# Kernel optimization log

Hardware: AMD Instinct MI355X
Metric: run time of the kernel (lower is better)

The kernel has to match this reference:

```python
import jax, jax.numpy as jnp
import numpy as np

N = 50000      # nodes
E = 800000     # directed edges
D = 128        # input_dim == hidden_dim
EL = 100000    # edges scored by decoder


def setup_inputs() -> dict:
    key = jax.random.key(0)
    ks = jax.random.split(key, 8)
    s = 1.0 / np.sqrt(D)  # glorot-ish scale
    return {
        "node_feature": jax.random.normal(ks[0], (N, D), jnp.float32),
        "W1": jax.random.normal(ks[1], (D, D), jnp.float32) * s,
        "b1": jnp.zeros((D,), jnp.float32),
        "W2": jax.random.normal(ks[2], (D, D), jnp.float32) * s,
        "b2": jnp.zeros((D,), jnp.float32),
        "W3": jax.random.normal(ks[3], (D, D), jnp.float32) * s,
        "b3": jnp.zeros((D,), jnp.float32),
        "edge_index": jax.random.randint(ks[4], (2, E), 0, N, dtype=jnp.int32),
        "edge_label_index": jax.random.randint(ks[5], (2, EL), 0, N, dtype=jnp.int32),
    }


def _gcn_conv(x, W, b, src, dst, norm, n):
    # x' = D^{-1/2} (A + I) D^{-1/2} (x W) + b   (PyG GCNConv semantics)
    h = x @ W                                   # [N, D]
    msg = h[src] * norm[:, None]                # gather + scale, [E+N, D]
    out = jax.ops.segment_sum(msg, dst, num_segments=n)  # scatter-add
    return out + b


def reference(node_feature, W1, b1, W2, b2, W3, b3, edge_index, edge_label_index):
    n = node_feature.shape[0]
    loop = jnp.arange(n, dtype=edge_index.dtype)
    src = jnp.concatenate([edge_index[0], loop])  # self-loops appended
    dst = jnp.concatenate([edge_index[1], loop])
    # symmetric normalization: deg over destinations (incl. self-loops)
    deg = jax.ops.segment_sum(jnp.ones_like(dst, dtype=node_feature.dtype), dst, num_segments=n)
    dinv = jax.lax.rsqrt(jnp.maximum(deg, 1.0))
    norm = dinv[src] * dinv[dst]                 # [E+N]

    x = jax.nn.relu(_gcn_conv(node_feature, W1, b1, src, dst, norm, n))
    x = jax.nn.relu(_gcn_conv(x, W2, b2, src, dst, norm, n))
    x = _gcn_conv(x, W3, b3, src, dst, norm, n)

    # dot-product edge decoder
    u = x[edge_label_index[0]]
    v = x[edge_label_index[1]]
    return jnp.sum(u * v, axis=-1)               # [EL] logits
```

## Files before the change

kernel.cpp:

```cpp
#include <hip/hip_runtime.h>
#include <hip/hip_bf16.h>
#include <hip/hip_fp16.h>

typedef _Float16 v8h __attribute__((ext_vector_type(8)));
typedef _Float16 v4h __attribute__((ext_vector_type(4)));
typedef float v4f __attribute__((ext_vector_type(4)));

__global__ __launch_bounds__(256) void wswz(const float* __restrict__ W1,
                                            const float* __restrict__ W2,
                                            const float* __restrict__ W3,
                                            __half* __restrict__ wfrag) {
    int o = blockIdx.x * 256 + threadIdx.x;
    int w = o >> 14, r = o & 16383;
    const float* Ws = (w >= 3) ? W3 : ((w == 2) ? W2 : W1);
    float v = Ws[r];
    __half h;
    if (w == 1) {
        __half hv = __float2half_rn(v);
        h = __float2half_rn(v - __half2float(hv));
    } else {
        h = __float2half_rn(v);
    }
    int k = r >> 7, ncol = r & 127;
    int c = ncol >> 4, nl = ncol & 15;
    int s = k >> 5, quad = (k >> 3) & 3, j = k & 7;
    int di = ((c * 4 + s) * 64 + quad * 16 + nl) * 8 + j;
    wfrag[(size_t)w * 16384 + di] = h;
}

__global__ __launch_bounds__(256) void gemm1_mfma(const float* __restrict__ X,
                                                  const __half* __restrict__ wfrag,
                                                  __half* __restrict__ H, int Nrows,
                                                  int degBlocks,
                                                  const int* __restrict__ dst,
                                                  int* __restrict__ cnt,
                                                  int* __restrict__ rank, int E) {
    int tid = threadIdx.x;
    if (blockIdx.x < degBlocks) {
        int base = blockIdx.x * 2048 + tid * 8;
        if (base + 7 < E) {
            int4 d0 = *(const int4*)&dst[base];
            int4 d1 = *(const int4*)&dst[base + 4];
            int r0 = atomicAdd(&cnt[d0.x * 16], 1);
            int r1 = atomicAdd(&cnt[d0.y * 16], 1);
            int r2 = atomicAdd(&cnt[d0.z * 16], 1);
            int r3 = atomicAdd(&cnt[d0.w * 16], 1);
            int r4 = atomicAdd(&cnt[d1.x * 16], 1);
            int r5 = atomicAdd(&cnt[d1.y * 16], 1);
            int r6 = atomicAdd(&cnt[d1.z * 16], 1);
            int r7 = atomicAdd(&cnt[d1.w * 16], 1);
            *(int4*)&rank[base]     = make_int4(r0, r1, r2, r3);
            *(int4*)&rank[base + 4] = make_int4(r4, r5, r6, r7);
        } else {
            for (int e = base; e < E; ++e) rank[e] = atomicAdd(&cnt[dst[e] * 16], 1);
        }
        return;
    }
    int gb = blockIdx.x - degBlocks;
    int rowbase = gb * 64;
    int l = tid & 63;
    int wid = tid >> 6;
    int rb = wid * 16;
    int quad = l >> 4;
    int nn = l & 15;
    int gr = rowbase + rb + nn;
    v8h ah[4], al[4];
    if (gr < Nrows) {
        const float* Xr = &X[(size_t)gr * 128 + quad * 8];
#pragma unroll
        for (int k = 0; k < 4; ++k) {
            float4 f0 = *(const float4*)&Xr[k * 32];
            float4 f1 = *(const float4*)&Xr[k * 32 + 4];
            float ff[8] = {f0.x, f0.y, f0.z, f0.w, f1.x, f1.y, f1.z, f1.w};
            v8h h, lo;
#pragma unroll
            for (int m = 0; m < 8; ++m) {
                _Float16 hv = (_Float16)ff[m];
                h[m] = hv;
                lo[m] = (_Float16)(ff[m] - (float)hv);
            }
            ah[k] = h;
            al[k] = lo;
        }
    } else {
#pragma unroll
        for (int k = 0; k < 4; ++k) {
            v8h z;
#pragma unroll
            for (int m = 0; m < 8; ++m) z[m] = (_Float16)0.f;
            ah[k] = z;
            al[k] = z;
        }
    }
    const v8h* Wh = (const v8h*)wfrag;
    const v8h* Wl = (const v8h*)(wfrag + 16384);
    v4f acc[8] = {};
#pragma unroll
    for (int c = 0; c < 8; ++c) {
        v8h bh0 = Wh[(c * 4 + 0) * 64 + l];
        v8h bh1 = Wh[(c * 4 + 1) * 64 + l];
        v8h bh2 = Wh[(c * 4 + 2) * 64 + l];
        v8h bh3 = Wh[(c * 4 + 3) * 64 + l];
        acc[c] = __builtin_amdgcn_mfma_f32_16x16x32_f16(ah[0], bh0, acc[c], 0, 0, 0);
        acc[c] = __builtin_amdgcn_mfma_f32_16x16x32_f16(ah[1], bh1, acc[c], 0, 0, 0);
        acc[c] = __builtin_amdgcn_mfma_f32_16x16x32_f16(ah[2], bh2, acc[c], 0, 0, 0);
        acc[c] = __builtin_amdgcn_mfma_f32_16x16x32_f16(ah[3], bh3, acc[c], 0, 0, 0);
        acc[c] = __builtin_amdgcn_mfma_f32_16x16x32_f16(al[0], bh0, acc[c], 0, 0, 0);
        acc[c] = __builtin_amdgcn_mfma_f32_16x16x32_f16(al[1], bh1, acc[c], 0, 0, 0);
        acc[c] = __builtin_amdgcn_mfma_f32_16x16x32_f16(al[2], bh2, acc[c], 0, 0, 0);
        acc[c] = __builtin_amdgcn_mfma_f32_16x16x32_f16(al[3], bh3, acc[c], 0, 0, 0);
        v8h bl0 = Wl[(c * 4 + 0) * 64 + l];
        v8h bl1 = Wl[(c * 4 + 1) * 64 + l];
        v8h bl2 = Wl[(c * 4 + 2) * 64 + l];
        v8h bl3 = Wl[(c * 4 + 3) * 64 + l];
        acc[c] = __builtin_amdgcn_mfma_f32_16x16x32_f16(ah[0], bl0, acc[c], 0, 0, 0);
        acc[c] = __builtin_amdgcn_mfma_f32_16x16x32_f16(ah[1], bl1, acc[c], 0, 0, 0);
        acc[c] = __builtin_amdgcn_mfma_f32_16x16x32_f16(ah[2], bl2, acc[c], 0, 0, 0);
        acc[c] = __builtin_amdgcn_mfma_f32_16x16x32_f16(ah[3], bl3, acc[c], 0, 0, 0);
    }
#pragma unroll
    for (int reg = 0; reg < 4; ++reg) {
        int grr = rowbase + rb + quad * 4 + reg;
        if (grr < Nrows) {
#pragma unroll
            for (int c = 0; c < 8; ++c)
                H[(size_t)grr * 128 + c * 16 + nn] = __float2half_rn(acc[c][reg]);
        }
    }
}

__global__ __launch_bounds__(256) void agg_gemm(const __half* __restrict__ Xs,
                                                const float* __restrict__ dinv,
                                                const int* __restrict__ rowptr,
                                                const int* __restrict__ col,
                                                const __half* __restrict__ wfrag,
                                                const float* __restrict__ bias,
                                                __half* __restrict__ Out,
                                                int n, int finalLayer) {
    __shared__ __align__(16) _Float16 y[64][136];
    int tid = threadIdx.x;
    int rowbase = blockIdx.x * 64;
    {
        int sub = tid >> 4;
        int t = (tid & 15) * 8;
        for (int g = 0; g < 4; ++g) {
            int rr = g * 16 + sub;
            int node = rowbase + rr;
            float a[8] = {};
            if (node < n) {
                int beg = rowptr[node], end = rowptr[node + 1];
                int k = beg;
                for (; k + 4 <= end; k += 4) {
                    int s0 = col[k], s1 = col[k + 1], s2 = col[k + 2], s3 = col[k + 3];
                    uint4 r0 = *(const uint4*)&Xs[(size_t)s0 * 128 + t];
                    uint4 r1 = *(const uint4*)&Xs[(size_t)s1 * 128 + t];
                    uint4 r2 = *(const uint4*)&Xs[(size_t)s2 * 128 + t];
                    uint4 r3 = *(const uint4*)&Xs[(size_t)s3 * 128 + t];
                    const __half2* h0 = (const __half2*)&r0;
                    const __half2* h1 = (const __half2*)&r1;
                    const __half2* h2 = (const __half2*)&r2;
                    const __half2* h3 = (const __half2*)&r3;
#pragma unroll
                    for (int m = 0; m < 4; ++m) {
                        float2 f0 = __half22float2(h0[m]);
                        float2 f1 = __half22float2(h1[m]);
                        float2 f2 = __half22float2(h2[m]);
                        float2 f3 = __half22float2(h3[m]);
                        a[2 * m]     += (f0.x + f1.x) + (f2.x + f3.x);
                        a[2 * m + 1] += (f0.y + f1.y) + (f2.y + f3.y);
                    }
                }
                for (; k < end; ++k) {
                    uint4 r0 = *(const uint4*)&Xs[(size_t)col[k] * 128 + t];
                    const __half2* h0 = (const __half2*)&r0;
#pragma unroll
                    for (int m = 0; m < 4; ++m) {
                        float2 f0 = __half22float2(h0[m]);
                        a[2 * m] += f0.x;
                        a[2 * m + 1] += f0.y;
                    }
                }
                float dn = dinv[node];
#pragma unroll
                for (int m = 0; m < 8; ++m) a[m] *= dn;
            }
            v8h yv;
#pragma unroll
            for (int m = 0; m < 8; ++m) yv[m] = (_Float16)a[m];
            *(v8h*)&y[rr][t] = yv;
        }
    }
    __syncthreads();
    int l = tid & 63;
    int wid = tid >> 6;
    int rb = wid * 16;
    int quad = l >> 4;
    int nn = l & 15;
    v8h a0 = *(const v8h*)&y[rb + nn][0 * 32 + quad * 8];
    v8h a1 = *(const v8h*)&y[rb + nn][1 * 32 + quad * 8];
    v8h a2 = *(const v8h*)&y[rb + nn][2 * 32 + quad * 8];
    v8h a3 = *(const v8h*)&y[rb + nn][3 * 32 + quad * 8];
    const v8h* Wf = (const v8h*)wfrag;
    v4f acc[8] = {};
#pragma unroll
    for (int c = 0; c < 8; ++c) {
        v8h b0 = Wf[(c * 4 + 0) * 64 + l];
        v8h b1 = Wf[(c * 4 + 1) * 64 + l];
        v8h b2 = Wf[(c * 4 + 2) * 64 + l];
        v8h b3 = Wf[(c * 4 + 3) * 64 + l];
        acc[c] = __builtin_amdgcn_mfma_f32_16x16x32_f16(a0, b0, acc[c], 0, 0, 0);
        acc[c] = __builtin_amdgcn_mfma_f32_16x16x32_f16(a1, b1, acc[c], 0, 0, 0);
        acc[c] = __builtin_amdgcn_mfma_f32_16x16x32_f16(a2, b2, acc[c], 0, 0, 0);
        acc[c] = __builtin_amdgcn_mfma_f32_16x16x32_f16(a3, b3, acc[c], 0, 0, 0);
    }
#pragma unroll
    for (int reg = 0; reg < 4; ++reg) {
        int gr = rowbase + rb + quad * 4 + reg;
        if (gr < n) {
            float dn = dinv[gr];
#pragma unroll
            for (int c = 0; c < 8; ++c) {
                float z = acc[c][reg] + bias[c * 16 + nn];
                if (!finalLayer) z = fmaxf(z, 0.f) * dn;
                Out[(size_t)gr * 128 + c * 16 + nn] = __float2half_rn(z);
            }
        }
    }
}

__global__ void scanA(const int* __restrict__ cnt, int* __restrict__ tmp,
                      int* __restrict__ bsum, int n) {
    __shared__ int s[256];
    int i = blockIdx.x * 256 + threadIdx.x;
    int v = (i < n) ? (cnt[i * 16] + 1) : 0;
    s[threadIdx.x] = v;
    __syncthreads();
    for (int off = 1; off < 256; off <<= 1) {
        int x = (threadIdx.x >= off) ? s[threadIdx.x - off] : 0;
        __syncthreads();
        s[threadIdx.x] += x;
        __syncthreads();
    }
    if (i < n) tmp[i] = s[threadIdx.x];
    if (threadIdx.x == 255) bsum[blockIdx.x] = s[255];
}

__global__ void scanB(const int* __restrict__ tmp, const int* __restrict__ bsum,
                      const int* __restrict__ cnt, int* __restrict__ rowptr,
                      float* __restrict__ dinv, int* __restrict__ col, int n, int nb) {
    __shared__ int p[256];
    int t = threadIdx.x;
    p[t] = (t < nb) ? bsum[t] : 0;
    __syncthreads();
    for (int off = 1; off < 256; off <<= 1) {
        int x = (t >= off) ? p[t - off] : 0;
        __syncthreads();
        p[t] += x;
        __syncthreads();
    }
    int prefix = (blockIdx.x == 0) ? 0 : p[blockIdx.x - 1];
    int i = blockIdx.x * 256 + t;
    if (i < n) {
        int inc = tmp[i] + prefix;
        rowptr[i + 1] = inc;
        int c1 = cnt[i * 16] + 1;
        dinv[i] = rsqrtf((float)c1);
        col[inc - c1] = i;
        if (i == 0) rowptr[0] = 0;
    }
}

__global__ __launch_bounds__(256) void fill4(const int* __restrict__ src,
                                             const int* __restrict__ dst,
                                             const int* __restrict__ rank,
                                             const int* __restrict__ rowptr,
                                             int* __restrict__ col, int E) {
    int base = blockIdx.x * 1024 + threadIdx.x * 4;
    if (base + 3 < E) {
        int d0 = dst[base], d1 = dst[base + 1], d2 = dst[base + 2], d3 = dst[base + 3];
        int s0 = src[base], s1 = src[base + 1], s2 = src[base + 2], s3 = src[base + 3];
        int r0 = rank[base], r1 = rank[base + 1], r2 = rank[base + 2], r3 = rank[base + 3];
        col[rowptr[d0] + 1 + r0] = s0;
        col[rowptr[d1] + 1 + r1] = s1;
        col[rowptr[d2] + 1 + r2] = s2;
        col[rowptr[d3] + 1 + r3] = s3;
    } else {
        for (int e = base; e < E; ++e)
            col[rowptr[dst[e]] + 1 + rank[e]] = src[e];
    }
}

__global__ __launch_bounds__(256) void agg_h(const __half* __restrict__ H,
                                             const float* __restrict__ dinv,
                                             const int* __restrict__ rowptr,
                                             const int* __restrict__ col,
                                             const float* __restrict__ bias,
                                             __half* __restrict__ out, int n) {
    int node = blockIdx.x * 16 + (threadIdx.x >> 4);
    int t = (threadIdx.x & 15) * 8;
    if (node >= n) return;
    int beg = rowptr[node], end = rowptr[node + 1];
    float a[8] = {};
    int k = beg;
    for (; k + 4 <= end; k += 4) {
        int s0 = col[k], s1 = col[k + 1], s2 = col[k + 2], s3 = col[k + 3];
        float w0 = dinv[s0], w1 = dinv[s1], w2 = dinv[s2], w3 = dinv[s3];
        uint4 r0 = *(const uint4*)&H[(size_t)s0 * 128 + t];
        uint4 r1 = *(const uint4*)&H[(size_t)s1 * 128 + t];
        uint4 r2 = *(const uint4*)&H[(size_t)s2 * 128 + t];
        uint4 r3 = *(const uint4*)&H[(size_t)s3 * 128 + t];
        const __half2* h0 = (const __half2*)&r0;
        const __half2* h1 = (const __half2*)&r1;
        const __half2* h2 = (const __half2*)&r2;
        const __half2* h3 = (const __half2*)&r3;
#pragma unroll
        for (int m = 0; m < 4; ++m) {
            float2 f0 = __half22float2(h0[m]);
            float2 f1 = __half22float2(h1[m]);
            float2 f2 = __half22float2(h2[m]);
            float2 f3 = __half22float2(h3[m]);
            a[2 * m]     += f0.x * w0 + f1.x * w1 + f2.x * w2 + f3.x * w3;
            a[2 * m + 1] += f0.y * w0 + f1.y * w1 + f2.y * w2 + f3.y * w3;
        }
    }
    for (; k < end; ++k) {
        int s0 = col[k];
        float w0 = dinv[s0];
        uint4 r0 = *(const uint4*)&H[(size_t)s0 * 128 + t];
        const __half2* h0 = (const __half2*)&r0;
#pragma unroll
        for (int m = 0; m < 4; ++m) {
            float2 f0 = __half22float2(h0[m]);
            a[2 * m] += f0.x * w0;
            a[2 * m + 1] += f0.y * w0;
        }
    }
    float dn = dinv[node];
    float4 b0 = *(const float4*)&bias[t];
    float4 b1 = *(const float4*)&bias[t + 4];
    float r0 = fmaxf(a[0] * dn + b0.x, 0.f) * dn;
    float r1 = fmaxf(a[1] * dn + b0.y, 0.f) * dn;
    float r2 = fmaxf(a[2] * dn + b0.z, 0.f) * dn;
    float r3 = fmaxf(a[3] * dn + b0.w, 0.f) * dn;
    float r4 = fmaxf(a[4] * dn + b1.x, 0.f) * dn;
    float r5 = fmaxf(a[5] * dn + b1.y, 0.f) * dn;
    float r6 = fmaxf(a[6] * dn + b1.z, 0.f) * dn;
    float r7 = fmaxf(a[7] * dn + b1.w, 0.f) * dn;
    auto pk = [](float x, float y) { __half2 h = __floats2half2_rn(x, y); return *(unsigned int*)&h; };
    uint4 o = make_uint4(pk(r0, r1), pk(r2, r3), pk(r4, r5), pk(r6, r7));
    *(uint4*)&out[(size_t)node * 128 + t] = o;
}

__global__ __launch_bounds__(256) void decoder_h(const __half* __restrict__ X,
                                                 const int* __restrict__ eli,
                                                 float* __restrict__ out, int EL) {
    int e = blockIdx.x * 16 + (threadIdx.x >> 4);
    int lane = threadIdx.x & 15;
    if (e >= EL) return;
    int u = eli[e], v = eli[EL + e];
    uint4 ra = *(const uint4*)&X[(size_t)u * 128 + lane * 8];
    uint4 rb = *(const uint4*)&X[(size_t)v * 128 + lane * 8];
    const __half2* ha = (const __half2*)&ra;
    const __half2* hb = (const __half2*)&rb;
    float d = 0.f;
#pragma unroll
    for (int j = 0; j < 4; ++j) {
        float2 fa = __half22float2(ha[j]);
        float2 fb = __half22float2(hb[j]);
        d += fa.x * fb.x + fa.y * fb.y;
    }
#pragma unroll
    for (int off = 8; off > 0; off >>= 1) d += __shfl_xor(d, off);
    if (lane == 0) out[e] = d;
}

extern "C" void kernel_launch(void* const* d_in, const int* in_sizes, int n_in,
                              void* d_out, int out_size, void* d_ws, size_t ws_size,
                              hipStream_t stream) {
    const float* x0 = (const float*)d_in[0];
    const float* W1 = (const float*)d_in[1];
    const float* b1 = (const float*)d_in[2];
    const float* W2 = (const float*)d_in[3];
    const float* b2 = (const float*)d_in[4];
    const float* W3 = (const float*)d_in[5];
    const float* b3 = (const float*)d_in[6];
    const int* ei   = (const int*)d_in[7];
    const int* eli  = (const int*)d_in[8];
    float* out = (float*)d_out;

    const int D = 128;
    const int N  = in_sizes[0] / D;
    const int E  = in_sizes[7] / 2;
    const int EL = in_sizes[8] / 2;

    const int* src = ei;
    const int* dst = ei + E;

    char* ws = (char*)d_ws;
    size_t off = 0;
    auto alloc = [&](size_t bytes) -> void* {
        off = (off + 255) & ~(size_t)255;
        void* p = ws + off;
        off += bytes;
        return p;
    };
    int*    cnt    = (int*)alloc((size_t)N * 16 * sizeof(int));
    int*    tmp    = (int*)alloc((size_t)N * sizeof(int));
    int*    bsum   = (int*)alloc(256 * sizeof(int));
    int*    rowptr = (int*)alloc((size_t)(N + 1) * sizeof(int));
    float*  dinv   = (float*)alloc((size_t)N * sizeof(float));
    int*    rank   = (int*)alloc((size_t)E * sizeof(int));
    int*    col    = (int*)alloc((size_t)(E + N) * sizeof(int));
    __half* wfrag  = (__half*)alloc((size_t)4 * 16384 * sizeof(__half));
    __half* hbuf   = (__half*)alloc((size_t)N * D * sizeof(__half));
    __half* xbuf   = (__half*)alloc((size_t)N * D * sizeof(__half));
    (void)ws_size;

    hipMemsetAsync(cnt, 0, (size_t)N * 16 * sizeof(int), stream);

    int nbN = (N + 255) / 256;
    int nbE4 = (E + 1023) / 1024;
    int nbE8 = (E + 2047) / 2048;
    int gemmGrid = (N + 63) / 64;
    int fusedGrid = (N + 63) / 64;
    int aggGrid  = (N + 15) / 16;

    wswz<<<256, 256, 0, stream>>>(W1, W2, W3, wfrag);

    gemm1_mfma<<<nbE8 + gemmGrid, 256, 0, stream>>>(x0, wfrag, hbuf, N,
                                                    nbE8, dst, cnt, rank, E);

    scanA<<<nbN, 256, 0, stream>>>(cnt, tmp, bsum, N);
    scanB<<<nbN, 256, 0, stream>>>(tmp, bsum, cnt, rowptr, dinv, col, N, nbN);
    fill4<<<nbE4, 256, 0, stream>>>(src, dst, rank, rowptr, col, E);

    agg_h<<<aggGrid, 256, 0, stream>>>(hbuf, dinv, rowptr, col, b1, xbuf, N);
    agg_gemm<<<fusedGrid, 256, 0, stream>>>(xbuf, dinv, rowptr, col, wfrag + 2 * 16384, b2, hbuf, N, 0);
    agg_gemm<<<fusedGrid, 256, 0, stream>>>(hbuf, dinv, rowptr, col, wfrag + 3 * 16384, b3, xbuf, N, 1);

    decoder_h<<<(EL + 15) / 16, 256, 0, stream>>>(xbuf, eli, out, EL);
}
```

Baseline: 266.5 us.

## Use wavefront-per-node aggregation, compact degree counters, prefetch weight fragments

The aggregation kernels now assign a full 64-lane wavefront to each node, with each lane loading one half2 and the edge loop unrolled by 8. This replaces the previous scheme of 16 lanes per node with uint4 loads, aiming for more edge-level memory parallelism and better balance across node degrees. The degree counter array drops its 16-int padding, which shrinks the memset and the scan reads at the risk of more atomic contention within a cache line. The first GEMM also prefetches the next column group's high weight fragments while the current MFMAs run.

```diff
diff --git a/kernel.cpp b/kernel.cpp
--- a/kernel.cpp
+++ b/kernel.cpp
@@ -28,36 +28,35 @@
     wfrag[(size_t)w * 16384 + di] = h;
 }
 
-__global__ __launch_bounds__(256) void gemm1_mfma(const float* __restrict__ X,
-                                                  const __half* __restrict__ wfrag,
-                                                  __half* __restrict__ H, int Nrows,
-                                                  int degBlocks,
-                                                  const int* __restrict__ dst,
-                                                  int* __restrict__ cnt,
-                                                  int* __restrict__ rank, int E) {
+__global__ __launch_bounds__(256) void gemm1_deg(const float* __restrict__ X,
+                                                 const __half* __restrict__ wfrag,
+                                                 __half* __restrict__ H, int Nrows,
+                                                 int degBlocks,
+                                                 const int* __restrict__ dst,
+                                                 int* __restrict__ cnt,
+                                                 int* __restrict__ rank, int E) {
     int tid = threadIdx.x;
     if (blockIdx.x < degBlocks) {
         int base = blockIdx.x * 2048 + tid * 8;
         if (base + 7 < E) {
             int4 d0 = *(const int4*)&dst[base];
             int4 d1 = *(const int4*)&dst[base + 4];
-            int r0 = atomicAdd(&cnt[d0.x * 16], 1);
-            int r1 = atomicAdd(&cnt[d0.y * 16], 1);
-            int r2 = atomicAdd(&cnt[d0.z * 16], 1);
-            int r3 = atomicAdd(&cnt[d0.w * 16], 1);
-            int r4 = atomicAdd(&cnt[d1.x * 16], 1);
-            int r5 = atomicAdd(&cnt[d1.y * 16], 1);
-            int r6 = atomicAdd(&cnt[d1.z * 16], 1);
-            int r7 = atomicAdd(&cnt[d1.w * 16], 1);
+            int r0 = atomicAdd(&cnt[d0.x], 1);
+            int r1 = atomicAdd(&cnt[d0.y], 1);
+            int r2 = atomicAdd(&cnt[d0.z], 1);
+            int r3 = atomicAdd(&cnt[d0.w], 1);
+            int r4 = atomicAdd(&cnt[d1.x], 1);
+            int r5 = atomicAdd(&cnt[d1.y], 1);
+            int r6 = atomicAdd(&cnt[d1.z], 1);
+            int r7 = atomicAdd(&cnt[d1.w], 1);
             *(int4*)&rank[base]     = make_int4(r0, r1, r2, r3);
             *(int4*)&rank[base + 4] = make_int4(r4, r5, r6, r7);
         } else {
-            for (int e = base; e < E; ++e) rank[e] = atomicAdd(&cnt[dst[e] * 16], 1);
+            for (int e = base; e < E; ++e) rank[e] = atomicAdd(&cnt[dst[e]], 1);
         }
         return;
     }
-    int gb = blockIdx.x - degBlocks;
-    int rowbase = gb * 64;
+    int rowbase = (blockIdx.x - degBlocks) * 64;
     int l = tid & 63;
     int wid = tid >> 6;
     int rb = wid * 16;
@@ -95,12 +94,16 @@
     const v8h* Wh = (const v8h*)wfrag;
     const v8h* Wl = (const v8h*)(wfrag + 16384);
     v4f acc[8] = {};
+    v8h bh0 = Wh[0 * 64 + l];
+    v8h bh1 = Wh[1 * 64 + l];
+    v8h bh2 = Wh[2 * 64 + l];
+    v8h bh3 = Wh[3 * 64 + l];
 #pragma unroll
     for (int c = 0; c < 8; ++c) {
-        v8h bh0 = Wh[(c * 4 + 0) * 64 + l];
-        v8h bh1 = Wh[(c * 4 + 1) * 64 + l];
-        v8h bh2 = Wh[(c * 4 + 2) * 64 + l];
-        v8h bh3 = Wh[(c * 4 + 3) * 64 + l];
+        v8h bl0 = Wl[(c * 4 + 0) * 64 + l];
+        v8h bl1 = Wl[(c * 4 + 1) * 64 + l];
+        v8h bl2 = Wl[(c * 4 + 2) * 64 + l];
+        v8h bl3 = Wl[(c * 4 + 3) * 64 + l];
         acc[c] = __builtin_amdgcn_mfma_f32_16x16x32_f16(ah[0], bh0, acc[c], 0, 0, 0);
         acc[c] = __builtin_amdgcn_mfma_f32_16x16x32_f16(ah[1], bh1, acc[c], 0, 0, 0);
         acc[c] = __builtin_amdgcn_mfma_f32_16x16x32_f16(ah[2], bh2, acc[c], 0, 0, 0);
@@ -109,14 +112,18 @@
         acc[c] = __builtin_amdgcn_mfma_f32_16x16x32_f16(al[1], bh1, acc[c], 0, 0, 0);
         acc[c] = __builtin_amdgcn_mfma_f32_16x16x32_f16(al[2], bh2, acc[c], 0, 0, 0);
         acc[c] = __builtin_amdgcn_mfma_f32_16x16x32_f16(al[3], bh3, acc[c], 0, 0, 0);
-        v8h bl0 = Wl[(c * 4 + 0) * 64 + l];
-        v8h bl1 = Wl[(c * 4 + 1) * 64 + l];
-        v8h bl2 = Wl[(c * 4 + 2) * 64 + l];
-        v8h bl3 = Wl[(c * 4 + 3) * 64 + l];
+        v8h nh0, nh1, nh2, nh3;
+        if (c < 7) {
+            nh0 = Wh[((c + 1) * 4 + 0) * 64 + l];
+            nh1 = Wh[((c + 1) * 4 + 1) * 64 + l];
+            nh2 = Wh[((c + 1) * 4 + 2) * 64 + l];
+            nh3 = Wh[((c + 1) * 4 + 3) * 64 + l];
+        }
         acc[c] = __builtin_amdgcn_mfma_f32_16x16x32_f16(ah[0], bl0, acc[c], 0, 0, 0);
         acc[c] = __builtin_amdgcn_mfma_f32_16x16x32_f16(ah[1], bl1, acc[c], 0, 0, 0);
         acc[c] = __builtin_amdgcn_mfma_f32_16x16x32_f16(ah[2], bl2, acc[c], 0, 0, 0);
         acc[c] = __builtin_amdgcn_mfma_f32_16x16x32_f16(ah[3], bl3, acc[c], 0, 0, 0);
+        if (c < 7) { bh0 = nh0; bh1 = nh1; bh2 = nh2; bh3 = nh3; }
     }
 #pragma unroll
     for (int reg = 0; reg < 4; ++reg) {
@@ -140,59 +147,55 @@
     __shared__ __align__(16) _Float16 y[64][136];
     int tid = threadIdx.x;
     int rowbase = blockIdx.x * 64;
+    int lane = tid & 63;
+    int wid = tid >> 6;
     {
-        int sub = tid >> 4;
-        int t = (tid & 15) * 8;
-        for (int g = 0; g < 4; ++g) {
-            int rr = g * 16 + sub;
+        int t2 = lane * 2;
+        for (int g = 0; g < 16; ++g) {
+            int rr = wid * 16 + g;
             int node = rowbase + rr;
-            float a[8] = {};
+            float a0 = 0.f, a1 = 0.f;
             if (node < n) {
                 int beg = rowptr[node], end = rowptr[node + 1];
                 int k = beg;
-                for (; k + 4 <= end; k += 4) {
+                for (; k + 8 <= end; k += 8) {
                     int s0 = col[k], s1 = col[k + 1], s2 = col[k + 2], s3 = col[k + 3];
-                    uint4 r0 = *(const uint4*)&Xs[(size_t)s0 * 128 + t];
-                    uint4 r1 = *(const uint4*)&Xs[(size_t)s1 * 128 + t];
-                    uint4 r2 = *(const uint4*)&Xs[(size_t)s2 * 128 + t];
-                    uint4 r3 = *(const uint4*)&Xs[(size_t)s3 * 128 + t];
-                    const __half2* h0 = (const __half2*)&r0;
-                    const __half2* h1 = (const __half2*)&r1;
-                    const __half2* h2 = (const __half2*)&r2;
-                    const __half2* h3 = (const __half2*)&r3;
-#pragma unroll
-                    for (int m = 0; m < 4; ++m) {
-                        float2 f0 = __half22float2(h0[m]);
-                        float2 f1 = __half22float2(h1[m]);
-                        float2 f2 = __half22float2(h2[m]);
-                        float2 f3 = __half22float2(h3[m]);
-                        a[2 * m]     += (f0.x + f1.x) + (f2.x + f3.x);
-                        a[2 * m + 1] += (f0.y + f1.y) + (f2.y + f3.y);
-                    }
+                    int s4 = col[k + 4], s5 = col[k + 5], s6 = col[k + 6], s7 = col[k + 7];
+                    __half2 u0 = *(const __half2*)&Xs[(size_t)s0 * 128 + t2];
+                    __half2 u1 = *(const __half2*)&Xs[(size_t)s1 * 128 + t2];
+                    __half2 u2 = *(const __half2*)&Xs[(size_t)s2 * 128 + t2];
+                    __half2 u3 = *(const __half2*)&Xs[(size_t)s3 * 128 + t2];
+                    __half2 u4 = *(const __half2*)&Xs[(size_t)s4 * 128 + t2];
+                    __half2 u5 = *(const __half2*)&Xs[(size_t)s5 * 128 + t2];
+                    __half2 u6 = *(const __half2*)&Xs[(size_t)s6 * 128 + t2];
+                    __half2 u7 = *(const __half2*)&Xs[(size_t)s7 * 128 + t2];
+                    float2 f0 = __half22float2(u0);
+                    float2 f1 = __half22float2(u1);
+                    float2 f2 = __half22float2(u2);
+                    float2 f3 = __half22float2(u3);
+                    float2 f4 = __half22float2(u4);
+                    float2 f5 = __half22float2(u5);
+                    float2 f6 = __half22float2(u6);
+                    float2 f7 = __half22float2(u7);
+                    a0 += ((f0.x + f1.x) + (f2.x + f3.x)) + ((f4.x + f5.x) + (f6.x + f7.x));
+                    a1 += ((f0.y + f1.y) + (f2.y + f3.y)) + ((f4.y + f5.y) + (f6.y + f7.y));
                 }
                 for (; k < end; ++k) {
-                    uint4 r0 = *(const uint4*)&Xs[(size_t)col[k] * 128 + t];
-                    const __half2* h0 = (const __half2*)&r0;
-#pragma unroll
-                    for (int m = 0; m < 4; ++m) {
-                        float2 f0 = __half22float2(h0[m]);
-                        a[2 * m] += f0.x;
-                        a[2 * m + 1] += f0.y;
-                    }
+                    __half2 u0 = *(const __half2*)&Xs[(size_t)col[k] * 128 + t2];
+                    float2 f0 = __half22float2(u0);
+                    a0 += f0.x;
+                    a1 += f0.y;
                 }
                 float dn = dinv[node];
-#pragma unroll
-                for (int m = 0; m < 8; ++m) a[m] *= dn;
+                a0 *= dn;
+                a1 *= dn;
             }
-            v8h yv;
-#pragma unroll
-            for (int m = 0; m < 8; ++m) yv[m] = (_Float16)a[m];
-            *(v8h*)&y[rr][t] = yv;
+            __half2 hv = __floats2half2_rn(a0, a1);
+            *(__half2*)&y[rr][t2] = hv;
         }
     }
     __syncthreads();
-    int l = tid & 63;
-    int wid = tid >> 6;
+    int l = lane;
     int rb = wid * 16;
     int quad = l >> 4;
     int nn = l & 15;
@@ -232,7 +235,7 @@
                       int* __restrict__ bsum, int n) {
     __shared__ int s[256];
     int i = blockIdx.x * 256 + threadIdx.x;
-    int v = (i < n) ? (cnt[i * 16] + 1) : 0;
+    int v = (i < n) ? (cnt[i] + 1) : 0;
     s[threadIdx.x] = v;
     __syncthreads();
     for (int off = 1; off < 256; off <<= 1) {
@@ -263,7 +266,7 @@
     if (i < n) {
         int inc = tmp[i] + prefix;
         rowptr[i + 1] = inc;
-        int c1 = cnt[i * 16] + 1;
+        int c1 = cnt[i] + 1;
         dinv[i] = rsqrtf((float)c1);
         col[inc - c1] = i;
         if (i == 0) rowptr[0] = 0;
@@ -296,59 +299,58 @@
                                              const int* __restrict__ col,
                                              const float* __restrict__ bias,
                                              __half* __restrict__ out, int n) {
-    int node = blockIdx.x * 16 + (threadIdx.x >> 4);
-    int t = (threadIdx.x & 15) * 8;
-    if (node >= n) return;
-    int beg = rowptr[node], end = rowptr[node + 1];
-    float a[8] = {};
-    int k = beg;
-    for (; k + 4 <= end; k += 4) {
-        int s0 = col[k], s1 = col[k + 1], s2 = col[k + 2], s3 = col[k + 3];
-        float w0 = dinv[s0], w1 = dinv[s1], w2 = dinv[s2], w3 = dinv[s3];
-        uint4 r0 = *(const uint4*)&H[(size_t)s0 * 128 + t];
-        uint4 r1 = *(const uint4*)&H[(size_t)s1 * 128 + t];
-        uint4 r2 = *(const uint4*)&H[(size_t)s2 * 128 + t];
-        uint4 r3 = *(const uint4*)&H[(size_t)s3 * 128 + t];
-        const __half2* h0 = (const __half2*)&r0;
-        const __half2* h1 = (const __half2*)&r1;
-        const __half2* h2 = (const __half2*)&r2;
-        const __half2* h3 = (const __half2*)&r3;
-#pragma unroll
-        for (int m = 0; m < 4; ++m) {
-            float2 f0 = __half22float2(h0[m]);
-            float2 f1 = __half22float2(h1[m]);
-            float2 f2 = __half22float2(h2[m]);
-            float2 f3 = __half22float2(h3[m]);
-            a[2 * m]     += f0.x * w0 + f1.x * w1 + f2.x * w2 + f3.x * w3;
-            a[2 * m + 1] += f0.y * w0 + f1.y * w1 + f2.y * w2 + f3.y * w3;
-        }
-    }
-    for (; k < end; ++k) {
-        int s0 = col[k];
-        float w0 = dinv[s0];
-        uint4 r0 = *(const uint4*)&H[(size_t)s0 * 128 + t];
-        const __half2* h0 = (const __half2*)&r0;
-#pragma unroll
-        for (int m = 0; m < 4; ++m) {
-            float2 f0 = __half22float2(h0[m]);
-            a[2 * m] += f0.x * w0;
-            a[2 * m + 1] += f0.y * w0;
-        }
-    }
-    float dn = dinv[node];
-    float4 b0 = *(const float4*)&bias[t];
-    float4 b1 = *(const float4*)&bias[t + 4];
-    float r0 = fmaxf(a[0] * dn + b0.x, 0.f) * dn;
-    float r1 = fmaxf(a[1] * dn + b0.y, 0.f) * dn;
-    float r2 = fmaxf(a[2] * dn + b0.z, 0.f) * dn;
-    float r3 = fmaxf(a[3] * dn + b0.w, 0.f) * dn;
-    float r4 = fmaxf(a[4] * dn + b1.x, 0.f) * dn;
-    float r5 = fmaxf(a[5] * dn + b1.y, 0.f) * dn;
-    float r6 = fmaxf(a[6] * dn + b1.z, 0.f) * dn;
-    float r7 = fmaxf(a[7] * dn + b1.w, 0.f) * dn;
-    auto pk = [](float x, float y) { __half2 h = __floats2half2_rn(x, y); return *(unsigned int*)&h; };
-    uint4 o = make_uint4(pk(r0, r1), pk(r2, r3), pk(r4, r5), pk(r6, r7));
-    *(uint4*)&out[(size_t)node * 128 + t] = o;
+    int tid = threadIdx.x;
+    int lane = tid & 63;
+    int wid = tid >> 6;
+    int t2 = lane * 2;
+    float2 bb = *(const float2*)&bias[t2];
+    int nodebase = blockIdx.x * 64 + wid * 16;
+    for (int g = 0; g < 16; ++g) {
+        int node = nodebase + g;
+        if (node >= n) return;
+        int beg = rowptr[node], end = rowptr[node + 1];
+        float a0 = 0.f, a1 = 0.f;
+        int k = beg;
+        for (; k + 8 <= end; k += 8) {
+            int s0 = col[k], s1 = col[k + 1], s2 = col[k + 2], s3 = col[k + 3];
+            int s4 = col[k + 4], s5 = col[k + 5], s6 = col[k + 6], s7 = col[k + 7];
+            float w0 = dinv[s0], w1 = dinv[s1], w2 = dinv[s2], w3 = dinv[s3];
+            float w4 = dinv[s4], w5 = dinv[s5], w6 = dinv[s6], w7 = dinv[s7];
+            __half2 u0 = *(const __half2*)&H[(size_t)s0 * 128 + t2];
+            __half2 u1 = *(const __half2*)&H[(size_t)s1 * 128 + t2];
+            __half2 u2 = *(const __half2*)&H[(size_t)s2 * 128 + t2];
+            __half2 u3 = *(const __half2*)&H[(size_t)s3 * 128 + t2];
+            __half2 u4 = *(const __half2*)&H[(size_t)s4 * 128 + t2];
+            __half2 u5 = *(const __half2*)&H[(size_t)s5 * 128 + t2];
+            __half2 u6 = *(const __half2*)&H[(size_t)s6 * 128 + t2];
+            __half2 u7 = *(const __half2*)&H[(size_t)s7 * 128 + t2];
+            float2 f0 = __half22float2(u0);
+            float2 f1 = __half22float2(u1);
+            float2 f2 = __half22float2(u2);
+            float2 f3 = __half22float2(u3);
+            float2 f4 = __half22float2(u4);
+            float2 f5 = __half22float2(u5);
+            float2 f6 = __half22float2(u6);
+            float2 f7 = __half22float2(u7);
+            a0 += (f0.x * w0 + f1.x * w1 + f2.x * w2 + f3.x * w3)
+                + (f4.x * w4 + f5.x * w5 + f6.x * w6 + f7.x * w7);
+            a1 += (f0.y * w0 + f1.y * w1 + f2.y * w2 + f3.y * w3)
+                + (f4.y * w4 + f5.y * w5 + f6.y * w6 + f7.y * w7);
+        }
+        for (; k < end; ++k) {
+            int s0 = col[k];
+            float w0 = dinv[s0];
+            __half2 u0 = *(const __half2*)&H[(size_t)s0 * 128 + t2];
+            float2 f0 = __half22float2(u0);
+            a0 += f0.x * w0;
+            a1 += f0.y * w0;
+        }
+        float dn = dinv[node];
+        float r0 = fmaxf(a0 * dn + bb.x, 0.f) * dn;
+        float r1 = fmaxf(a1 * dn + bb.y, 0.f) * dn;
+        __half2 o = __floats2half2_rn(r0, r1);
+        *(__half2*)&out[(size_t)node * 128 + t2] = o;
+    }
 }
 
 __global__ __launch_bounds__(256) void decoder_h(const __half* __restrict__ X,
@@ -404,7 +406,7 @@
         off += bytes;
         return p;
     };
-    int*    cnt    = (int*)alloc((size_t)N * 16 * sizeof(int));
+    int*    cnt    = (int*)alloc((size_t)N * sizeof(int));
     int*    tmp    = (int*)alloc((size_t)N * sizeof(int));
     int*    bsum   = (int*)alloc(256 * sizeof(int));
     int*    rowptr = (int*)alloc((size_t)(N + 1) * sizeof(int));
@@ -416,25 +418,24 @@
     __half* xbuf   = (__half*)alloc((size_t)N * D * sizeof(__half));
     (void)ws_size;
 
-    hipMemsetAsync(cnt, 0, (size_t)N * 16 * sizeof(int), stream);
+    hipMemsetAsync(cnt, 0, (size_t)N * sizeof(int), stream);
 
     int nbN = (N + 255) / 256;
     int nbE4 = (E + 1023) / 1024;
     int nbE8 = (E + 2047) / 2048;
     int gemmGrid = (N + 63) / 64;
     int fusedGrid = (N + 63) / 64;
-    int aggGrid  = (N + 15) / 16;
 
     wswz<<<256, 256, 0, stream>>>(W1, W2, W3, wfrag);
 
-    gemm1_mfma<<<nbE8 + gemmGrid, 256, 0, stream>>>(x0, wfrag, hbuf, N,
-                                                    nbE8, dst, cnt, rank, E);
+    gemm1_deg<<<nbE8 + gemmGrid, 256, 0, stream>>>(x0, wfrag, hbuf, N,
+                                                   nbE8, dst, cnt, rank, E);
 
     scanA<<<nbN, 256, 0, stream>>>(cnt, tmp, bsum, N);
     scanB<<<nbN, 256, 0, stream>>>(tmp, bsum, cnt, rowptr, dinv, col, N, nbN);
     fill4<<<nbE4, 256, 0, stream>>>(src, dst, rank, rowptr, col, E);
 
-    agg_h<<<aggGrid, 256, 0, stream>>>(hbuf, dinv, rowptr, col, b1, xbuf, N);
+    agg_h<<<fusedGrid, 256, 0, stream>>>(hbuf, dinv, rowptr, col, b1, xbuf, N);
     agg_gemm<<<fusedGrid, 256, 0, stream>>>(xbuf, dinv, rowptr, col, wfrag + 2 * 16384, b2, hbuf, N, 0);
     agg_gemm<<<fusedGrid, 256, 0, stream>>>(hbuf, dinv, rowptr, col, wfrag + 3 * 16384, b3, xbuf, N, 1);
 
```

After: 376.8 us. 41.4% more time.

## Widen agg_gemm to 512 threads, split output columns, prefetch gemm1 weights

Applied to the files above, without the earlier changes.

The fused aggregate+GEMM kernel now launches 512 threads per 64-row block. Each thread gathers 2 rows instead of 4, and each wave computes half of the output column chunks, which increases parallelism for the latency-bound gather. gemm1 now software-pipelines the high-part weight fragment loads one column chunk ahead, and agg_h gains an occupancy hint. The costs are more register pressure in gemm1 and duplicated A-fragment reads from shared memory in agg_gemm.

```diff
diff --git a/kernel.cpp b/kernel.cpp
--- a/kernel.cpp
+++ b/kernel.cpp
@@ -28,13 +28,13 @@
     wfrag[(size_t)w * 16384 + di] = h;
 }
 
-__global__ __launch_bounds__(256) void gemm1_mfma(const float* __restrict__ X,
-                                                  const __half* __restrict__ wfrag,
-                                                  __half* __restrict__ H, int Nrows,
-                                                  int degBlocks,
-                                                  const int* __restrict__ dst,
-                                                  int* __restrict__ cnt,
-                                                  int* __restrict__ rank, int E) {
+__global__ __launch_bounds__(256) void gemm1_deg(const float* __restrict__ X,
+                                                 const __half* __restrict__ wfrag,
+                                                 __half* __restrict__ H, int Nrows,
+                                                 int degBlocks,
+                                                 const int* __restrict__ dst,
+                                                 int* __restrict__ cnt,
+                                                 int* __restrict__ rank, int E) {
     int tid = threadIdx.x;
     if (blockIdx.x < degBlocks) {
         int base = blockIdx.x * 2048 + tid * 8;
@@ -56,8 +56,7 @@
         }
         return;
     }
-    int gb = blockIdx.x - degBlocks;
-    int rowbase = gb * 64;
+    int rowbase = (blockIdx.x - degBlocks) * 64;
     int l = tid & 63;
     int wid = tid >> 6;
     int rb = wid * 16;
@@ -95,12 +94,16 @@
     const v8h* Wh = (const v8h*)wfrag;
     const v8h* Wl = (const v8h*)(wfrag + 16384);
     v4f acc[8] = {};
+    v8h bh0 = Wh[0 * 64 + l];
+    v8h bh1 = Wh[1 * 64 + l];
+    v8h bh2 = Wh[2 * 64 + l];
+    v8h bh3 = Wh[3 * 64 + l];
 #pragma unroll
     for (int c = 0; c < 8; ++c) {
-        v8h bh0 = Wh[(c * 4 + 0) * 64 + l];
-        v8h bh1 = Wh[(c * 4 + 1) * 64 + l];
-        v8h bh2 = Wh[(c * 4 + 2) * 64 + l];
-        v8h bh3 = Wh[(c * 4 + 3) * 64 + l];
+        v8h bl0 = Wl[(c * 4 + 0) * 64 + l];
+        v8h bl1 = Wl[(c * 4 + 1) * 64 + l];
+        v8h bl2 = Wl[(c * 4 + 2) * 64 + l];
+        v8h bl3 = Wl[(c * 4 + 3) * 64 + l];
         acc[c] = __builtin_amdgcn_mfma_f32_16x16x32_f16(ah[0], bh0, acc[c], 0, 0, 0);
         acc[c] = __builtin_amdgcn_mfma_f32_16x16x32_f16(ah[1], bh1, acc[c], 0, 0, 0);
         acc[c] = __builtin_amdgcn_mfma_f32_16x16x32_f16(ah[2], bh2, acc[c], 0, 0, 0);
@@ -109,14 +112,18 @@
         acc[c] = __builtin_amdgcn_mfma_f32_16x16x32_f16(al[1], bh1, acc[c], 0, 0, 0);
         acc[c] = __builtin_amdgcn_mfma_f32_16x16x32_f16(al[2], bh2, acc[c], 0, 0, 0);
         acc[c] = __builtin_amdgcn_mfma_f32_16x16x32_f16(al[3], bh3, acc[c], 0, 0, 0);
-        v8h bl0 = Wl[(c * 4 + 0) * 64 + l];
-        v8h bl1 = Wl[(c * 4 + 1) * 64 + l];
-        v8h bl2 = Wl[(c * 4 + 2) * 64 + l];
-        v8h bl3 = Wl[(c * 4 + 3) * 64 + l];
+        v8h nh0, nh1, nh2, nh3;
+        if (c < 7) {
+            nh0 = Wh[((c + 1) * 4 + 0) * 64 + l];
+            nh1 = Wh[((c + 1) * 4 + 1) * 64 + l];
+            nh2 = Wh[((c + 1) * 4 + 2) * 64 + l];
+            nh3 = Wh[((c + 1) * 4 + 3) * 64 + l];
+        }
         acc[c] = __builtin_amdgcn_mfma_f32_16x16x32_f16(ah[0], bl0, acc[c], 0, 0, 0);
         acc[c] = __builtin_amdgcn_mfma_f32_16x16x32_f16(ah[1], bl1, acc[c], 0, 0, 0);
         acc[c] = __builtin_amdgcn_mfma_f32_16x16x32_f16(ah[2], bl2, acc[c], 0, 0, 0);
         acc[c] = __builtin_amdgcn_mfma_f32_16x16x32_f16(ah[3], bl3, acc[c], 0, 0, 0);
+        if (c < 7) { bh0 = nh0; bh1 = nh1; bh2 = nh2; bh3 = nh3; }
     }
 #pragma unroll
     for (int reg = 0; reg < 4; ++reg) {
@@ -129,22 +136,22 @@
     }
 }
 
-__global__ __launch_bounds__(256) void agg_gemm(const __half* __restrict__ Xs,
-                                                const float* __restrict__ dinv,
-                                                const int* __restrict__ rowptr,
-                                                const int* __restrict__ col,
-                                                const __half* __restrict__ wfrag,
-                                                const float* __restrict__ bias,
-                                                __half* __restrict__ Out,
-                                                int n, int finalLayer) {
+__global__ __launch_bounds__(512, 8) void agg_gemm(const __half* __restrict__ Xs,
+                                                   const float* __restrict__ dinv,
+                                                   const int* __restrict__ rowptr,
+                                                   const int* __restrict__ col,
+                                                   const __half* __restrict__ wfrag,
+                                                   const float* __restrict__ bias,
+                                                   __half* __restrict__ Out,
+                                                   int n, int finalLayer) {
     __shared__ __align__(16) _Float16 y[64][136];
     int tid = threadIdx.x;
     int rowbase = blockIdx.x * 64;
     {
-        int sub = tid >> 4;
+        int grp = tid >> 4;
         int t = (tid & 15) * 8;
-        for (int g = 0; g < 4; ++g) {
-            int rr = g * 16 + sub;
+        for (int g = 0; g < 2; ++g) {
+            int rr = g * 32 + grp;
             int node = rowbase + rr;
             float a[8] = {};
             if (node < n) {
@@ -193,7 +200,8 @@
     __syncthreads();
     int l = tid & 63;
     int wid = tid >> 6;
-    int rb = wid * 16;
+    int rb = (wid >> 1) * 16;
+    int ch = wid & 1;
     int quad = l >> 4;
     int nn = l & 15;
     v8h a0 = *(const v8h*)&y[rb + nn][0 * 32 + quad * 8];
@@ -201,13 +209,14 @@
     v8h a2 = *(const v8h*)&y[rb + nn][2 * 32 + quad * 8];
     v8h a3 = *(const v8h*)&y[rb + nn][3 * 32 + quad * 8];
     const v8h* Wf = (const v8h*)wfrag;
-    v4f acc[8] = {};
-#pragma unroll
-    for (int c = 0; c < 8; ++c) {
-        v8h b0 = Wf[(c * 4 + 0) * 64 + l];
-        v8h b1 = Wf[(c * 4 + 1) * 64 + l];
-        v8h b2 = Wf[(c * 4 + 2) * 64 + l];
-        v8h b3 = Wf[(c * 4 + 3) * 64 + l];
+    v4f acc[4] = {};
+#pragma unroll
+    for (int c = 0; c < 4; ++c) {
+        int cc = ch * 4 + c;
+        v8h b0 = Wf[(cc * 4 + 0) * 64 + l];
+        v8h b1 = Wf[(cc * 4 + 1) * 64 + l];
+        v8h b2 = Wf[(cc * 4 + 2) * 64 + l];
+        v8h b3 = Wf[(cc * 4 + 3) * 64 + l];
         acc[c] = __builtin_amdgcn_mfma_f32_16x16x32_f16(a0, b0, acc[c], 0, 0, 0);
         acc[c] = __builtin_amdgcn_mfma_f32_16x16x32_f16(a1, b1, acc[c], 0, 0, 0);
         acc[c] = __builtin_amdgcn_mfma_f32_16x16x32_f16(a2, b2, acc[c], 0, 0, 0);
@@ -219,10 +228,11 @@
         if (gr < n) {
             float dn = dinv[gr];
 #pragma unroll
-            for (int c = 0; c < 8; ++c) {
-                float z = acc[c][reg] + bias[c * 16 + nn];
+            for (int c = 0; c < 4; ++c) {
+                int cc = ch * 4 + c;
+                float z = acc[c][reg] + bias[cc * 16 + nn];
                 if (!finalLayer) z = fmaxf(z, 0.f) * dn;
-                Out[(size_t)gr * 128 + c * 16 + nn] = __float2half_rn(z);
+                Out[(size_t)gr * 128 + cc * 16 + nn] = __float2half_rn(z);
             }
         }
     }
@@ -290,12 +300,12 @@
     }
 }
 
-__global__ __launch_bounds__(256) void agg_h(const __half* __restrict__ H,
-                                             const float* __restrict__ dinv,
-                                             const int* __restrict__ rowptr,
-                                             const int* __restrict__ col,
-                                             const float* __restrict__ bias,
-                                             __half* __restrict__ out, int n) {
+__global__ __launch_bounds__(256, 8) void agg_h(const __half* __restrict__ H,
+                                                const float* __restrict__ dinv,
+                                                const int* __restrict__ rowptr,
+                                                const int* __restrict__ col,
+                                                const float* __restrict__ bias,
+                                                __half* __restrict__ out, int n) {
     int node = blockIdx.x * 16 + (threadIdx.x >> 4);
     int t = (threadIdx.x & 15) * 8;
     if (node >= n) return;
@@ -427,16 +437,16 @@
 
     wswz<<<256, 256, 0, stream>>>(W1, W2, W3, wfrag);
 
-    gemm1_mfma<<<nbE8 + gemmGrid, 256, 0, stream>>>(x0, wfrag, hbuf, N,
-                                                    nbE8, dst, cnt, rank, E);
+    gemm1_deg<<<nbE8 + gemmGrid, 256, 0, stream>>>(x0, wfrag, hbuf, N,
+                                                   nbE8, dst, cnt, rank, E);
 
     scanA<<<nbN, 256, 0, stream>>>(cnt, tmp, bsum, N);
     scanB<<<nbN, 256, 0, stream>>>(tmp, bsum, cnt, rowptr, dinv, col, N, nbN);
     fill4<<<nbE4, 256, 0, stream>>>(src, dst, rank, rowptr, col, E);
 
     agg_h<<<aggGrid, 256, 0, stream>>>(hbuf, dinv, rowptr, col, b1, xbuf, N);
-    agg_gemm<<<fusedGrid, 256, 0, stream>>>(xbuf, dinv, rowptr, col, wfrag + 2 * 16384, b2, hbuf, N, 0);
-    agg_gemm<<<fusedGrid, 256, 0, stream>>>(hbuf, dinv, rowptr, col, wfrag + 3 * 16384, b3, xbuf, N, 1);
+    agg_gemm<<<fusedGrid, 512, 0, stream>>>(xbuf, dinv, rowptr, col, wfrag + 2 * 16384, b2, hbuf, N, 0);
+    agg_gemm<<<fusedGrid, 512, 0, stream>>>(hbuf, dinv, rowptr, col, wfrag + 3 * 16384, b3, xbuf, N, 1);
 
     decoder_h<<<(EL + 15) / 16, 256, 0, stream>>>(xbuf, eli, out, EL);
 }
```

Result: faster. 258.1 us (-3.2%).
